# Kernel optimization log

Hardware: AMD Instinct MI355X
Metric: run time of the kernel (lower is better)

## Reference

```python
import jax, jax.numpy as jnp
import numpy as np

D_EMBED = 64      # per-head dim (module uses d_embed as head dim)
N_HEADS = 8
SCALE = 1.0 / float(np.sqrt(D_EMBED))
ROPE_BASE = 10000.0


def _rope(x):
    # torchtune-style interleaved RoPE. x: [B, S, H, D]
    B, S, H, D = x.shape
    freqs = 1.0 / (ROPE_BASE ** (jnp.arange(0, D, 2, dtype=jnp.float32) / D))  # [D/2]
    ang = jnp.arange(S, dtype=jnp.float32)[:, None] * freqs[None, :]           # [S, D/2]
    cos = jnp.cos(ang)[None, :, None, :]
    sin = jnp.sin(ang)[None, :, None, :]
    x1 = x[..., 0::2]
    x2 = x[..., 1::2]
    return jnp.stack([x1 * cos - x2 * sin, x1 * sin + x2 * cos], axis=-1).reshape(B, S, H, D)


def setup_inputs() -> dict:
    key = jax.random.key(0)
    ks = jax.random.split(key, 5)
    B, S, D, H = 2, 2048, D_EMBED, N_HEADS
    std = 1.0 / np.sqrt(D)
    return {
        "q": jax.random.normal(ks[0], (B, S, D), jnp.float32),
        "Wq": jax.random.normal(ks[1], (H * D, D), jnp.float32) * std,
        "Wk": jax.random.normal(ks[2], (H * D, D), jnp.float32) * std,
        "Wv": jax.random.normal(ks[3], (H * D, D), jnp.float32) * std,
        "Wo": jax.random.normal(ks[4], (D, H * D), jnp.float32) * std,
        "gamma": jnp.ones((H,), jnp.float32),
    }


def reference(q, Wq, Wk, Wv, Wo, gamma):
    B, S, D = q.shape
    H = N_HEADS
    qh = (q @ Wq.T).reshape(B, S, H, D)
    kh = (q @ Wk.T).reshape(B, S, H, D)
    vh = (q @ Wv.T).reshape(B, S, H, D)
    qh = _rope(qh).transpose(0, 2, 1, 3)  # [B,H,S,D]
    kh = _rope(kh).transpose(0, 2, 1, 3)
    vh = vh.transpose(0, 2, 1, 3)
    # RBF attention scores
    qn = jnp.sum(qh * qh, axis=-1, keepdims=True)                 # [B,H,S,1]
    kn = jnp.sum(kh * kh, axis=-1, keepdims=True)                 # [B,H,S,1]
    qk = jnp.einsum('bhsd,bhtd->bhst', qh, kh)                    # [B,H,S,S]
    dist = jnp.maximum(qn - 2.0 * qk + jnp.swapaxes(kn, -2, -1), 0.0)
    scores = jnp.exp(-(gamma[None, :, None, None] * SCALE) * dist)
    causal = jnp.tril(jnp.ones((S, S), dtype=bool))
    scores = jnp.where(causal, scores, 0.0)
    out = jnp.einsum('bhst,bhtd->bhsd', scores, vh)
    out = out.transpose(0, 2, 1, 3).reshape(B, S, H * D)
    return out @ Wo.T
```

## Files before the change

kernel.cpp:

```cpp
#include <hip/hip_runtime.h>
#include <hip/hip_bf16.h>

#define BB 2
#define SS 2048
#define DD 64
#define HH 8
#define HD 512
#define SCALE 0.125f

typedef __bf16 bf16;
typedef __attribute__((ext_vector_type(4))) __bf16 bf16x4;
typedef __attribute__((ext_vector_type(8))) __bf16 bf16x8;
typedef __attribute__((ext_vector_type(4))) float floatx4;

#define PSLOT 2097152

__device__ __forceinline__ floatx4 mfma16(bf16x8 a, bf16x8 b, floatx4 c) {
    return __builtin_amdgcn_mfma_f32_16x16x32_bf16(a, b, c, 0, 0, 0);
}

#define PV_MFMA(ACC, A, B) \
    asm("s_nop 1\n\tv_mfma_f32_16x16x16_bf16 %0, %1, %2, %0" \
        : "+v"(ACC) : "v"(A), "v"(B))

#define MFMA_DRAIN4(A0, A1, A2, A3) \
    asm volatile("s_nop 7\n\ts_nop 7" : "+v"(A0), "+v"(A1), "+v"(A2), "+v"(A3))

#define GLL(G, L) __builtin_amdgcn_global_load_lds( \
    (const __attribute__((address_space(1))) void*)(G), \
    (__attribute__((address_space(3))) void*)(L), 16, 0, 0)

__device__ __forceinline__ bf16x8 load8(const void* base, size_t idx, int f32) {
    if (f32) {
        const float* p = (const float*)base + idx;
        const float4 a = *reinterpret_cast<const float4*>(p);
        const float4 b = *reinterpret_cast<const float4*>(p + 4);
        bf16x8 r;
        r[0] = (bf16)a.x; r[1] = (bf16)a.y; r[2] = (bf16)a.z; r[3] = (bf16)a.w;
        r[4] = (bf16)b.x; r[5] = (bf16)b.y; r[6] = (bf16)b.z; r[7] = (bf16)b.w;
        return r;
    }
    return *reinterpret_cast<const bf16x8*>((const bf16*)base + idx);
}

__device__ __forceinline__ float load1(const void* base, int idx, int f32) {
    return f32 ? ((const float*)base)[idx] : (float)((const bf16*)base)[idx];
}

__global__ __launch_bounds__(256) void proj_rope_kernel(
    const void* __restrict__ q, const void* __restrict__ Wq,
    const void* __restrict__ Wk, const void* __restrict__ Wv,
    bf16* __restrict__ qh, bf16* __restrict__ kh, bf16* __restrict__ vt,
    float* __restrict__ qn, float* __restrict__ kn,
    int* __restrict__ flagw)
{
    const int lane = threadIdx.x & 63;
    const int wid  = blockIdx.x * 4 + (threadIdx.x >> 6);
    if (wid >= 3 * BB * HH * (SS / 64)) return;
    const int l16  = lane & 15;
    const int quad = lane >> 4;

    int hit = 0;
    const unsigned short* qu = (const unsigned short*)q;
#pragma unroll
    for (int i = 0; i < 16; ++i) {
        const unsigned short u = qu[lane + i * 64];
        if (((u >> 7) & 0xFF) >= 134) hit = 1;
    }
    const int f32 = (__ballot(hit) != 0ull) ? 1 : 0;
    if (wid == 0 && lane == 0) *flagw = f32;

    int id = wid;
    const int h   = id % HH; id /= HH;
    const int st4 = id % (SS / 64); id /= (SS / 64);
    const int b   = id % BB; id /= BB;
    const int w   = id;

    const void* W = (w == 0) ? Wq : (w == 1) ? Wk : Wv;
    const size_t bh = (size_t)b * HH + h;

    bf16x8 wb0[4], wb1[4];
#pragma unroll
    for (int t = 0; t < 4; ++t) {
        const size_t wrow = (size_t)(h * 64 + t * 16 + l16) * DD;
        wb0[t] = load8(W, wrow + quad * 8, f32);
        wb1[t] = load8(W, wrow + quad * 8 + 32, f32);
    }

    float frevA[4], frevB[4];
    if (w < 2) {
#pragma unroll
        for (int t = 0; t < 4; ++t) {
            const int dbase = t * 16 + quad * 4;
            frevA[t] = __builtin_amdgcn_exp2f(
                -(float)dbase * (13.2877123795f / 64.0f)) * 0.15915494309f;
            frevB[t] = __builtin_amdgcn_exp2f(
                -(float)(dbase + 2) * (13.2877123795f / 64.0f)) * 0.15915494309f;
        }
    }

    for (int s4 = 0; s4 < 4; ++s4) {
        const int s0 = (st4 * 4 + s4) * 16;
        const size_t qrow = ((size_t)b * SS + s0 + l16) * DD;
        bf16x8 a0 = load8(q, qrow + quad * 8, f32);
        bf16x8 a1 = load8(q, qrow + quad * 8 + 32, f32);

        floatx4 cv[4];
#pragma unroll
        for (int t = 0; t < 4; ++t) {
            floatx4 acc = {0.f, 0.f, 0.f, 0.f};
            if (w < 2) {
                acc = mfma16(wb0[t], a0, acc);
                acc = mfma16(wb1[t], a1, acc);
            } else {
                acc = mfma16(a0, wb0[t], acc);
                acc = mfma16(a1, wb1[t], acc);
            }
            cv[t] = acc;
        }

        if (w < 2) {
            bf16*  dst  = (w == 0) ? qh : kh;
            float* ndst = (w == 0) ? qn : kn;
            const float srowf = (float)(s0 + l16);
            float nacc = 0.f;
            bf16* drow = dst + (bh * SS + s0 + l16) * DD + quad * 4;
#pragma unroll
            for (int t = 0; t < 4; ++t) {
                float revA = srowf * frevA[t]; revA -= floorf(revA);
                float revB = srowf * frevB[t]; revB -= floorf(revB);
                const float snA = __builtin_amdgcn_sinf(revA);
                const float csA = __builtin_amdgcn_cosf(revA);
                const float snB = __builtin_amdgcn_sinf(revB);
                const float csB = __builtin_amdgcn_cosf(revB);
                const float x0 = cv[t][0], x1 = cv[t][1];
                const float x2 = cv[t][2], x3 = cv[t][3];
                const float r0 = x0 * csA - x1 * snA;
                const float r1 = x0 * snA + x1 * csA;
                const float r2 = x2 * csB - x3 * snB;
                const float r3 = x2 * snB + x3 * csB;
                nacc += r0 * r0 + r1 * r1 + r2 * r2 + r3 * r3;
                bf16x4 o; o[0]=(bf16)r0; o[1]=(bf16)r1; o[2]=(bf16)r2; o[3]=(bf16)r3;
                *reinterpret_cast<bf16x4*>(drow + t * 16) = o;
            }
            nacc += __shfl_xor(nacc, 16);
            nacc += __shfl_xor(nacc, 32);
            if (quad == 0) ndst[bh * SS + s0 + l16] = nacc;
        } else {
            bf16* vrow = vt + ((size_t)bh * 128 + st4 * 4 + s4) * 1024
                       + l16 * 16 + quad * 4;
#pragma unroll
            for (int t = 0; t < 4; ++t) {
                bf16x4 pv;
#pragma unroll
                for (int r = 0; r < 4; ++r) pv[r] = (bf16)cv[t][r];
                *reinterpret_cast<bf16x4*>(vrow + t * 256) = pv;
            }
        }
    }
}

__global__ __launch_bounds__(256) void attn_kernel(
    const bf16* __restrict__ qh, const bf16* __restrict__ kh,
    const bf16* __restrict__ vt, const float* __restrict__ qn,
    const float* __restrict__ kn, const void* __restrict__ gamma,
    bf16* __restrict__ partial, const int* __restrict__ flagp,
    int ksh, int pb)
{
    __shared__ __align__(16) char smem[16384];
    const int f32  = *flagp;
    const int tid  = threadIdx.x;
    const int wv   = tid >> 6;
    const int lane = tid & 63;
    const int l16  = lane & 15;
    const int quad = lane >> 4;

    const int xcd  = blockIdx.x & 7;
    int sblk = blockIdx.x >> 3;
    const int half = (sblk >= pb) ? 1 : 0;
    const int bh   = xcd + (half << 3);
    sblk -= half * pb;
    int q4 = 0;
    for (;;) {
        const int ns = ((q4 * 64 + 63) >> ksh) + 1;
        if (sblk < ns) break;
        sblk -= ns; ++q4;
    }
    const int slot = sblk;
    const int qt   = q4 * 4 + wv;
    const int s0   = qt * 16;
    const int tb   = slot << ksh;
    const int te   = min(tb + (1 << ksh), (q4 + 1) * 64);
    const int nch  = (te - tb) >> 5;
    const int h    = bh & 7;

    const float cc = load1(gamma, h, f32) * SCALE * 1.4426950408889634f;

    const bf16* qbase = qh + ((size_t)bh * SS + s0 + l16) * DD;
    bf16x8 aq0 = *reinterpret_cast<const bf16x8*>(qbase + quad * 8);
    bf16x8 aq1 = *reinterpret_cast<const bf16x8*>(qbase + quad * 8 + 32);
    const float qn_l = qn[(size_t)bh * SS + s0 + l16];

    floatx4 acc0 = {0.f,0.f,0.f,0.f}, acc1 = {0.f,0.f,0.f,0.f};
    floatx4 acc2 = {0.f,0.f,0.f,0.f}, acc3 = {0.f,0.f,0.f,0.f};

    const float* knp   = kn + (size_t)bh * SS + quad * 4;
    const char* kgbase = (const char*)(kh + (size_t)bh * SS * DD);
    const char* vgbase = (const char*)(vt + (size_t)bh * 131072);

    const int jK   = wv * 64 + lane;
    const int keyK = jK >> 3;
    const int cK   = ((jK & 7) - keyK) & 7;
    const int goffK = keyK * 128 + cK * 16;
    const int goffV = jK * 16;
    char* ldsK = smem + wv * 1024;
    char* ldsV = smem + 8192 + wv * 1024;

    const int kro0 = (l16 * 8 + ((quad + l16) & 7)) * 16;
    const int kro1 = (l16 * 8 + ((quad + 4 + l16) & 7)) * 16;
    const int vro  = l16 * 32 + quad * 8;

    GLL(kgbase + (size_t)tb * 128 + goffK, ldsK);
    GLL(vgbase + (size_t)(tb >> 4) * 2048 + goffV, ldsV);
    __syncthreads();

    int buf = 0, t0 = tb;
    for (int c = 0; c < nch; ++c, t0 += 32) {
        if (c + 1 < nch) {
            GLL(kgbase + (size_t)(t0 + 32) * 128 + goffK, ldsK + ((buf ^ 1) << 12));
            GLL(vgbase + (size_t)((t0 + 32) >> 4) * 2048 + goffV, ldsV + ((buf ^ 1) << 12));
        }
        const float4 knv0 = *reinterpret_cast<const float4*>(knp + t0);
        const float4 knv1 = *reinterpret_cast<const float4*>(knp + t0 + 16);
        const char* Kb = smem + (buf << 12);
        const char* Vb = smem + 8192 + (buf << 12);

        bf16x8 kc0 = *reinterpret_cast<const bf16x8*>(Kb + kro0);
        bf16x8 kc1 = *reinterpret_cast<const bf16x8*>(Kb + kro1);
        bf16x8 kc2 = *reinterpret_cast<const bf16x8*>(Kb + 2048 + kro0);
        bf16x8 kc3 = *reinterpret_cast<const bf16x8*>(Kb + 2048 + kro1);
        bf16x4 v00 = *reinterpret_cast<const bf16x4*>(Vb + vro);
        bf16x4 v01 = *reinterpret_cast<const bf16x4*>(Vb + 512 + vro);
        bf16x4 v02 = *reinterpret_cast<const bf16x4*>(Vb + 1024 + vro);
        bf16x4 v03 = *reinterpret_cast<const bf16x4*>(Vb + 1536 + vro);
        bf16x4 v10 = *reinterpret_cast<const bf16x4*>(Vb + 2048 + vro);
        bf16x4 v11 = *reinterpret_cast<const bf16x4*>(Vb + 2560 + vro);
        bf16x4 v12 = *reinterpret_cast<const bf16x4*>(Vb + 3072 + vro);
        bf16x4 v13 = *reinterpret_cast<const bf16x4*>(Vb + 3584 + vro);

        floatx4 z0 = {0.f,0.f,0.f,0.f};
        z0 = mfma16(kc0, aq0, z0);
        z0 = mfma16(kc1, aq1, z0);
        floatx4 z1 = {0.f,0.f,0.f,0.f};
        z1 = mfma16(kc2, aq0, z1);
        z1 = mfma16(kc3, aq1, z1);

        const float* k0_ = (const float*)&knv0;
        const float* k1_ = (const float*)&knv1;
        bf16x4 p0, p1;
        if (t0 + 31 <= s0) {
#pragma unroll
            for (int i = 0; i < 4; ++i) {
                float rawA = fmaf(-2.f, z0[i], qn_l + k0_[i]);
                float rawB = fmaf(-2.f, z1[i], qn_l + k1_[i]);
                p0[i] = (bf16)__builtin_amdgcn_exp2f(fminf(-cc * rawA, 0.f));
                p1[i] = (bf16)__builtin_amdgcn_exp2f(fminf(-cc * rawB, 0.f));
            }
        } else {
            const int dq0 = s0 + l16 - t0 - quad * 4;
            const int dq1 = dq0 - 16;
#pragma unroll
            for (int i = 0; i < 4; ++i) {
                float rawA = fmaf(-2.f, z0[i], qn_l + k0_[i]);
                float rawB = fmaf(-2.f, z1[i], qn_l + k1_[i]);
                float eA = __builtin_amdgcn_exp2f(fminf(-cc * rawA, 0.f));
                float eB = __builtin_amdgcn_exp2f(fminf(-cc * rawB, 0.f));
                p0[i] = (bf16)((i <= dq0) ? eA : 0.f);
                p1[i] = (bf16)((i <= dq1) ? eB : 0.f);
            }
        }

        PV_MFMA(acc0, v00, p0);
        PV_MFMA(acc1, v01, p0);
        PV_MFMA(acc2, v02, p0);
        PV_MFMA(acc3, v03, p0);
        PV_MFMA(acc0, v10, p1);
        PV_MFMA(acc1, v11, p1);
        PV_MFMA(acc2, v12, p1);
        PV_MFMA(acc3, v13, p1);

        __syncthreads();
        buf ^= 1;
    }

    MFMA_DRAIN4(acc0, acc1, acc2, acc3);

    bf16* pbp = partial + (size_t)slot * PSLOT
              + ((size_t)bh * SS + s0 + l16) * DD + quad * 4;
    bf16x4 o;
#define STORE4(PTR, ACC) \
    o[0]=(bf16)(ACC)[0]; o[1]=(bf16)(ACC)[1]; o[2]=(bf16)(ACC)[2]; o[3]=(bf16)(ACC)[3]; \
    *reinterpret_cast<bf16x4*>(PTR) = o;
    STORE4(pbp +  0, acc0)
    STORE4(pbp + 16, acc1)
    STORE4(pbp + 32, acc2)
    STORE4(pbp + 48, acc3)
#undef STORE4
}

template <int NACT>
__device__ __forceinline__ floatx4 opj_core(const bf16* __restrict__ partial,
                                            const void* __restrict__ Wo,
                                            int b, int srow, size_t brow,
                                            int f32, int quad) {
    floatx4 acc = {0.f, 0.f, 0.f, 0.f};
#pragma unroll 4
    for (int kk = 0; kk < HD; kk += 32) {
        const int h  = kk >> 6;
        const int d0 = (kk & 63) + quad * 8;
        const bf16* ap = partial + (((size_t)(b * 8 + h)) * SS + srow) * 64 + d0;
        bf16x8 v0 = *reinterpret_cast<const bf16x8*>(ap);
        float u[8];
#pragma unroll
        for (int i = 0; i < 8; ++i) u[i] = (float)v0[i];
#pragma unroll
        for (int s = 1; s < NACT; ++s) {
            bf16x8 vs = *reinterpret_cast<const bf16x8*>(ap + (size_t)s * PSLOT);
#pragma unroll
            for (int i = 0; i < 8; ++i) u[i] += (float)vs[i];
        }
        bf16x8 a;
#pragma unroll
        for (int i = 0; i < 8; ++i) a[i] = (bf16)u[i];
        bf16x8 w = load8(Wo, brow + kk, f32);
        acc = mfma16(a, w, acc);
    }
    return acc;
}

__global__ __launch_bounds__(256) void outproj_kernel(
    const bf16* __restrict__ partial, const void* __restrict__ Wo,
    void* __restrict__ out, const int* __restrict__ flagp, int ksh)
{
    const int f32  = *flagp;
    const int ct   = threadIdx.x >> 6;
    const int lane = threadIdx.x & 63;
    const int l16  = lane & 15;
    const int quad = lane >> 4;

    const int g0   = blockIdx.x * 16;
    const int b    = g0 >> 11;
    const int s0   = g0 & (SS - 1);
    const int nact = (s0 >> ksh) + 1;
    const int srow = s0 + l16;
    const size_t brow = (size_t)(ct * 16 + l16) * HD + quad * 8;

    floatx4 acc;
    switch (nact) {
        case 1:  acc = opj_core<1>(partial, Wo, b, srow, brow, f32, quad); break;
        case 2:  acc = opj_core<2>(partial, Wo, b, srow, brow, f32, quad); break;
        case 3:  acc = opj_core<3>(partial, Wo, b, srow, brow, f32, quad); break;
        default: acc = opj_core<4>(partial, Wo, b, srow, brow, f32, quad); break;
    }

#pragma unroll
    for (int r = 0; r < 4; ++r) {
        const size_t o = (size_t)(g0 + quad * 4 + r) * DD + ct * 16 + l16;
        if (f32) ((float*)out)[o] = acc[r];
        else     ((bf16*)out)[o]  = (bf16)acc[r];
    }
}

extern "C" void kernel_launch(void* const* d_in, const int* in_sizes, int n_in,
                              void* d_out, int out_size, void* d_ws, size_t ws_size,
                              hipStream_t stream) {
    const void* q     = d_in[0];
    const void* Wq    = d_in[1];
    const void* Wk    = d_in[2];
    const void* Wv    = d_in[3];
    const void* Wo    = d_in[4];
    const void* gamma = d_in[5];

    char* ws = (char*)d_ws;
    bf16*  qh      = (bf16*)(ws);
    bf16*  kh      = (bf16*)(ws + 4194304);
    bf16*  vt      = (bf16*)(ws + 8388608);
    float* qn      = (float*)(ws + 12582912);
    float* kn      = (float*)(ws + 12713984);
    int*   flag    = (int*)  (ws + 12845056);
    bf16*  partial = (bf16*)(ws + 13631488);

    int ksh = 11;
    const size_t base = 13631488ull;
    if (ws_size >= base + 2ull * 4194304) ksh = 10;

    int pb = 0;
    for (int q4 = 0; q4 < 32; ++q4) pb += ((q4 * 64 + 63) >> ksh) + 1;

    const int nproj = 3 * BB * HH * (SS / 64);
    proj_rope_kernel<<<dim3((nproj + 3) / 4), dim3(256), 0, stream>>>(
        q, Wq, Wk, Wv, qh, kh, vt, qn, kn, flag);
    attn_kernel<<<dim3(16 * pb), dim3(256), 0, stream>>>(
        qh, kh, vt, qn, kn, gamma, partial, flag, ksh, pb);
    outproj_kernel<<<dim3(BB * SS / 16), dim3(256), 0, stream>>>(
        partial, Wo, d_out, flag, ksh);
}
```

Measured before the change: 120.1 us.

## Pair light and heavy causal query tiles into equal-length attention work units

Work decomposition changes from fixed key-range split-K slots to pairing query block j with block 31-j, so every workgroup processes the same number of 32-key chunks (66/NU) split across NU partial slots. The goal is to remove load imbalance from the causal triangle and the serial loop that mapped a block index to its tile. The output projection's partial-sum count per row is recomputed to match. A workgroup may now store an intermediate partial result mid-loop and reload its Q fragment, which adds some branch and register cost.

Result: faster. 115.6 us (-3.7%).

```diff
diff --git a/kernel.cpp b/kernel.cpp
--- a/kernel.cpp
+++ b/kernel.cpp
@@ -165,7 +165,7 @@
     const bf16* __restrict__ vt, const float* __restrict__ qn,
     const float* __restrict__ kn, const void* __restrict__ gamma,
     bf16* __restrict__ partial, const int* __restrict__ flagp,
-    int ksh, int pb)
+    int NU, int U, int pb)
 {
     __shared__ __align__(16) char smem[16384];
     const int f32  = *flagp;
@@ -180,26 +180,26 @@
     const int half = (sblk >= pb) ? 1 : 0;
     const int bh   = xcd + (half << 3);
     sblk -= half * pb;
-    int q4 = 0;
-    for (;;) {
-        const int ns = ((q4 * 64 + 63) >> ksh) + 1;
-        if (sblk < ns) break;
-        sblk -= ns; ++q4;
-    }
-    const int slot = sblk;
-    const int qt   = q4 * 4 + wv;
-    const int s0   = qt * 16;
-    const int tb   = slot << ksh;
-    const int te   = min(tb + (1 << ksh), (q4 + 1) * 64);
-    const int nch  = (te - tb) >> 5;
+
+    const int j   = sblk / NU;
+    const int u   = sblk - j * NU;
+    const int B   = 2 * (j + 1);
+    const int c0  = u * U;
+    const int nA  = (c0 < B) ? (((c0 + U) < B ? (c0 + U) : B) - c0) : 0;
+    const int bB  = ((c0 > B ? c0 : B) - B);
+    const int slotA = u;
+    const int slotB = u - (B / U);
     const int h    = bh & 7;
 
     const float cc = load1(gamma, h, f32) * SCALE * 1.4426950408889634f;
 
-    const bf16* qbase = qh + ((size_t)bh * SS + s0 + l16) * DD;
-    bf16x8 aq0 = *reinterpret_cast<const bf16x8*>(qbase + quad * 8);
-    bf16x8 aq1 = *reinterpret_cast<const bf16x8*>(qbase + quad * 8 + 32);
-    const float qn_l = qn[(size_t)bh * SS + s0 + l16];
+    int q4 = (nA > 0) ? j : (31 - j);
+    int s0 = (q4 * 4 + wv) * 16;
+
+    const bf16* qb = qh + ((size_t)bh * SS + s0 + l16) * DD;
+    bf16x8 aq0 = *reinterpret_cast<const bf16x8*>(qb + quad * 8);
+    bf16x8 aq1 = *reinterpret_cast<const bf16x8*>(qb + quad * 8 + 32);
+    float qn_l = qn[(size_t)bh * SS + s0 + l16];
 
     floatx4 acc0 = {0.f,0.f,0.f,0.f}, acc1 = {0.f,0.f,0.f,0.f};
     floatx4 acc2 = {0.f,0.f,0.f,0.f}, acc3 = {0.f,0.f,0.f,0.f};
@@ -220,16 +220,49 @@
     const int kro1 = (l16 * 8 + ((quad + 4 + l16) & 7)) * 16;
     const int vro  = l16 * 32 + quad * 8;
 
-    GLL(kgbase + (size_t)tb * 128 + goffK, ldsK);
-    GLL(vgbase + (size_t)(tb >> 4) * 2048 + goffV, ldsV);
+#define T0_OF(C) (((C) < nA ? (c0 + (C)) : (bB + (C) - nA)) * 32)
+
+#define STORE_O(SLOT, S0) do { \
+    bf16* pbp = partial + (size_t)(SLOT) * PSLOT \
+              + ((size_t)bh * SS + (S0) + l16) * DD + quad * 4; \
+    bf16x4 o_; \
+    o_[0]=(bf16)acc0[0]; o_[1]=(bf16)acc0[1]; o_[2]=(bf16)acc0[2]; o_[3]=(bf16)acc0[3]; \
+    *reinterpret_cast<bf16x4*>(pbp +  0) = o_; \
+    o_[0]=(bf16)acc1[0]; o_[1]=(bf16)acc1[1]; o_[2]=(bf16)acc1[2]; o_[3]=(bf16)acc1[3]; \
+    *reinterpret_cast<bf16x4*>(pbp + 16) = o_; \
+    o_[0]=(bf16)acc2[0]; o_[1]=(bf16)acc2[1]; o_[2]=(bf16)acc2[2]; o_[3]=(bf16)acc2[3]; \
+    *reinterpret_cast<bf16x4*>(pbp + 32) = o_; \
+    o_[0]=(bf16)acc3[0]; o_[1]=(bf16)acc3[1]; o_[2]=(bf16)acc3[2]; o_[3]=(bf16)acc3[3]; \
+    *reinterpret_cast<bf16x4*>(pbp + 48) = o_; \
+} while (0)
+
+    {
+        const int t0p = T0_OF(0);
+        GLL(kgbase + (size_t)t0p * 128 + goffK, ldsK);
+        GLL(vgbase + (size_t)(t0p >> 4) * 2048 + goffV, ldsV);
+    }
     __syncthreads();
 
-    int buf = 0, t0 = tb;
-    for (int c = 0; c < nch; ++c, t0 += 32) {
-        if (c + 1 < nch) {
-            GLL(kgbase + (size_t)(t0 + 32) * 128 + goffK, ldsK + ((buf ^ 1) << 12));
-            GLL(vgbase + (size_t)((t0 + 32) >> 4) * 2048 + goffV, ldsV + ((buf ^ 1) << 12));
-        }
+    int buf = 0;
+    for (int c = 0; c < U; ++c) {
+        if (c + 1 < U) {
+            const int tn = T0_OF(c + 1);
+            GLL(kgbase + (size_t)tn * 128 + goffK, ldsK + ((buf ^ 1) << 12));
+            GLL(vgbase + (size_t)(tn >> 4) * 2048 + goffV, ldsV + ((buf ^ 1) << 12));
+        }
+        if (c == nA && nA > 0) {
+            MFMA_DRAIN4(acc0, acc1, acc2, acc3);
+            STORE_O(slotA, s0);
+            acc0 = {0.f,0.f,0.f,0.f}; acc1 = {0.f,0.f,0.f,0.f};
+            acc2 = {0.f,0.f,0.f,0.f}; acc3 = {0.f,0.f,0.f,0.f};
+            q4 = 31 - j;
+            s0 = (q4 * 4 + wv) * 16;
+            const bf16* qb2 = qh + ((size_t)bh * SS + s0 + l16) * DD;
+            aq0 = *reinterpret_cast<const bf16x8*>(qb2 + quad * 8);
+            aq1 = *reinterpret_cast<const bf16x8*>(qb2 + quad * 8 + 32);
+            qn_l = qn[(size_t)bh * SS + s0 + l16];
+        }
+        const int t0 = T0_OF(c);
         const float4 knv0 = *reinterpret_cast<const float4*>(knp + t0);
         const float4 knv1 = *reinterpret_cast<const float4*>(knp + t0 + 16);
         const char* Kb = smem + (buf << 12);
@@ -294,18 +327,9 @@
     }
 
     MFMA_DRAIN4(acc0, acc1, acc2, acc3);
-
-    bf16* pbp = partial + (size_t)slot * PSLOT
-              + ((size_t)bh * SS + s0 + l16) * DD + quad * 4;
-    bf16x4 o;
-#define STORE4(PTR, ACC) \
-    o[0]=(bf16)(ACC)[0]; o[1]=(bf16)(ACC)[1]; o[2]=(bf16)(ACC)[2]; o[3]=(bf16)(ACC)[3]; \
-    *reinterpret_cast<bf16x4*>(PTR) = o;
-    STORE4(pbp +  0, acc0)
-    STORE4(pbp + 16, acc1)
-    STORE4(pbp + 32, acc2)
-    STORE4(pbp + 48, acc3)
-#undef STORE4
+    STORE_O((nA == U) ? slotA : slotB, s0);
+#undef STORE_O
+#undef T0_OF
 }
 
 template <int NACT>
@@ -340,7 +364,7 @@
 
 __global__ __launch_bounds__(256) void outproj_kernel(
     const bf16* __restrict__ partial, const void* __restrict__ Wo,
-    void* __restrict__ out, const int* __restrict__ flagp, int ksh)
+    void* __restrict__ out, const int* __restrict__ flagp, int NU, int U)
 {
     const int f32  = *flagp;
     const int ct   = threadIdx.x >> 6;
@@ -351,9 +375,13 @@
     const int g0   = blockIdx.x * 16;
     const int b    = g0 >> 11;
     const int s0   = g0 & (SS - 1);
-    const int nact = (s0 >> ksh) + 1;
     const int srow = s0 + l16;
     const size_t brow = (size_t)(ct * 16 + l16) * HD + quad * 8;
+
+    const int q4g = s0 >> 6;
+    int nact;
+    if (q4g < 16) { const int Bp = 2 * (q4g + 1); nact = (Bp + U - 1) / U; }
+    else          { const int Bp = 2 * (32 - q4g); nact = NU - Bp / U; }
 
     floatx4 acc;
     switch (nact) {
@@ -390,18 +418,16 @@
     int*   flag    = (int*)  (ws + 12845056);
     bf16*  partial = (bf16*)(ws + 13631488);
 
-    int ksh = 11;
     const size_t base = 13631488ull;
-    if (ws_size >= base + 2ull * 4194304) ksh = 10;
-
-    int pb = 0;
-    for (int q4 = 0; q4 < 32; ++q4) pb += ((q4 * 64 + 63) >> ksh) + 1;
+    int NU = (ws_size >= base + 3ull * 4194304) ? 3 : 2;
+    const int U  = 66 / NU;
+    const int pb = 16 * NU;
 
     const int nproj = 3 * BB * HH * (SS / 64);
     proj_rope_kernel<<<dim3((nproj + 3) / 4), dim3(256), 0, stream>>>(
         q, Wq, Wk, Wv, qh, kh, vt, qn, kn, flag);
     attn_kernel<<<dim3(16 * pb), dim3(256), 0, stream>>>(
-        qh, kh, vt, qn, kn, gamma, partial, flag, ksh, pb);
+        qh, kh, vt, qn, kn, gamma, partial, flag, NU, U, pb);
     outproj_kernel<<<dim3(BB * SS / 16), dim3(256), 0, stream>>>(
-        partial, Wo, d_out, flag, ksh);
-}
+        partial, Wo, d_out, flag, NU, U);
+}
```
